# Kernel tuning notes

Measured on AMD Instinct MI355X. Metric: run time of the kernel, lower is better.

Reference implementation:

```python
import jax, jax.numpy as jnp
import numpy as np

B, T, NW, NF = 4, 1, 1536, 16
N_CROSS = 400_000
N_EDGES = 1_600_000
C_OUT = 4
IN_DIM = 2 * NF + 2  # 34


def setup_inputs() -> dict:
    key = jax.random.key(0)
    ks = jax.random.split(key, 16)
    return {
        "first_wires": jax.random.normal(ks[0], (B, T, NW, NF), jnp.float32),
        "second_wires": jax.random.normal(ks[1], (B, T, NW, NF), jnp.float32),
        "crossings": jax.random.normal(ks[2], (N_CROSS, 2), jnp.float32),
        "bbox": jax.random.uniform(ks[3], (3,), jnp.float32) + 0.5,
        "edge_attr": jax.random.normal(ks[4], (N_EDGES, 4), jnp.float32),
        "indices": jax.random.randint(ks[5], (N_CROSS, 2), 0, NW),
        "edge_index": jax.random.randint(ks[6], (2, N_EDGES), 0, N_CROSS),
        "W": jax.random.normal(ks[7], (IN_DIM, C_OUT), jnp.float32) / np.sqrt(IN_DIM),
        "att_src": jax.random.normal(ks[8], (C_OUT,), jnp.float32),
        "att_dst": jax.random.normal(ks[9], (C_OUT,), jnp.float32),
        "W_e": jax.random.normal(ks[10], (4, C_OUT), jnp.float32) / 2.0,
        "att_edge": jax.random.normal(ks[11], (C_OUT,), jnp.float32),
        "bias": jnp.zeros((C_OUT,), jnp.float32),
        "w_mlp": jax.random.normal(ks[12], (C_OUT, 1), jnp.float32) / 2.0,
        "b_mlp": jnp.zeros((1,), jnp.float32),
    }


def reference(first_wires, second_wires, crossings, bbox, edge_attr,
              indices, edge_index, W, att_src, att_dst, W_e, att_edge,
              bias, w_mlp, b_mlp):
    b, t = first_wires.shape[0], first_wires.shape[1]
    n = indices.shape[0]
    # fill_window: gather wire features for each crossing and append normalized coords
    fw = first_wires[:, :, indices[:, 0], :]          # [B,T,N,NF]
    sw = second_wires[:, :, indices[:, 1], :]         # [B,T,N,NF]
    xc = crossings / jnp.linalg.norm(bbox)            # [N,2]
    xc = jnp.broadcast_to(xc[None, None], (b, t, n, 2))
    x = jnp.concatenate([fw, sw, xc], axis=-1)        # [B,T,N,2NF+2]
    x = x.reshape(b * t, n, -1)

    src, dst = edge_index[0], edge_index[1]
    h = x @ W                                          # [BT,N,C]
    a_e = (edge_attr @ W_e) @ att_edge                 # [E]

    def gat(hb):
        hs, hd = hb[src], hb[dst]                      # [E,C]
        logits = jax.nn.leaky_relu(hs @ att_src + hd @ att_dst + a_e, 0.2)
        m = jax.ops.segment_max(logits, dst, num_segments=n)
        ex = jnp.exp(logits - m[dst])
        den = jax.ops.segment_sum(ex, dst, num_segments=n)
        alpha = ex / (den[dst] + 1e-16)
        return jax.ops.segment_sum(alpha[:, None] * hs, dst, num_segments=n) + bias

    out = jax.vmap(gat)(h)                             # [BT,N,C]
    y = out @ w_mlp + b_mlp                            # [BT,N,1]
    return y.reshape(b, t, n, 1)
```

## Files before the change

### kernel.cpp

```cpp
#include <hip/hip_runtime.h>
#include <math.h>

#define BB 4
#define NWIRE 1536
#define NFEAT 16
#define BS 256
#define NBLK 256
#define DSHIFT 8
#define DPB (1 << DSHIFT)
#define MAXNB 2048

__global__ void k_wires(const float* __restrict__ fw, const float* __restrict__ sw,
                        const float* __restrict__ W, const float* __restrict__ att_src,
                        const float* __restrict__ att_dst, const float* __restrict__ wmlp,
                        float4* __restrict__ fwpre, float4* __restrict__ swpre) {
    int t = blockIdx.x * blockDim.x + threadIdx.x;
    if (t >= BB * NWIRE) return;
    const float* fp = fw + (size_t)t * NFEAT;
    const float* sp = sw + (size_t)t * NFEAT;
    float hf[4] = {0, 0, 0, 0}, hs[4] = {0, 0, 0, 0};
    #pragma unroll
    for (int k = 0; k < NFEAT; ++k) {
        float a = fp[k], b = sp[k];
        #pragma unroll
        for (int c = 0; c < 4; ++c) {
            hf[c] = fmaf(a, W[k * 4 + c], hf[c]);
            hs[c] = fmaf(b, W[(NFEAT + k) * 4 + c], hs[c]);
        }
    }
    float fs = 0, fd = 0, fq = 0, ss = 0, sd = 0, sq = 0;
    #pragma unroll
    for (int c = 0; c < 4; ++c) {
        float as = att_src[c], ad = att_dst[c], wm = wmlp[c];
        fs = fmaf(hf[c], as, fs); fd = fmaf(hf[c], ad, fd); fq = fmaf(hf[c], wm, fq);
        ss = fmaf(hs[c], as, ss); sd = fmaf(hs[c], ad, sd); sq = fmaf(hs[c], wm, sq);
    }
    fwpre[t] = make_float4(fs, fd, fq, 0.0f);
    swpre[t] = make_float4(ss, sd, sq, 0.0f);
}

__global__ void k_nodes(const int* __restrict__ indices, const float* __restrict__ crossings,
                        const float* __restrict__ bbox, const float* __restrict__ W,
                        const float* __restrict__ att_src, const float* __restrict__ att_dst,
                        const float* __restrict__ wmlp,
                        const float4* __restrict__ fwpre, const float4* __restrict__ swpre,
                        float4* __restrict__ srcdat4, float4* __restrict__ dstdat4, int n) {
    int i = blockIdx.x * blockDim.x + threadIdx.x;
    if (i >= n) return;
    float inv = rsqrtf(bbox[0] * bbox[0] + bbox[1] * bbox[1] + bbox[2] * bbox[2]);
    int2 idx = ((const int2*)indices)[i];
    float2 xc = ((const float2*)crossings)[i];
    int i0 = idx.x, i1 = idx.y;
    float x0 = xc.x * inv, x1 = xc.y * inv;
    float xs = 0, xd = 0, xq = 0;
    #pragma unroll
    for (int c = 0; c < 4; ++c) {
        float hc = fmaf(x0, W[32 * 4 + c], x1 * W[33 * 4 + c]);
        xs = fmaf(hc, att_src[c], xs);
        xd = fmaf(hc, att_dst[c], xd);
        xq = fmaf(hc, wmlp[c], xq);
    }
    float4 f0 = fwpre[0 * NWIRE + i0], s0 = swpre[0 * NWIRE + i1];
    float4 f1 = fwpre[1 * NWIRE + i0], s1 = swpre[1 * NWIRE + i1];
    float4 f2 = fwpre[2 * NWIRE + i0], s2 = swpre[2 * NWIRE + i1];
    float4 f3 = fwpre[3 * NWIRE + i0], s3 = swpre[3 * NWIRE + i1];
    srcdat4[(size_t)i * 2] = make_float4(f0.x + s0.x + xs, f1.x + s1.x + xs,
                                         f2.x + s2.x + xs, f3.x + s3.x + xs);
    srcdat4[(size_t)i * 2 + 1] = make_float4(f0.z + s0.z + xq, f1.z + s1.z + xq,
                                             f2.z + s2.z + xq, f3.z + s3.z + xq);
    dstdat4[i] = make_float4(f0.y + s0.y + xd, f1.y + s1.y + xd,
                             f2.y + s2.y + xd, f3.y + s3.y + xd);
}

__global__ void k_binA1(const int* __restrict__ ei, int ne, int nb, int chunk,
                        int* __restrict__ bh) {
    __shared__ int lc[MAXNB];
    for (int i = threadIdx.x; i < nb; i += BS) lc[i] = 0;
    __syncthreads();
    int blk = blockIdx.x;
    const int* dstp = ei + ne;
    int e0 = blk * chunk, e1 = min(e0 + chunk, ne);
    int e = e0 + threadIdx.x * 4;
    for (; e + 3 < e1; e += BS * 4) {
        int4 d4 = *(const int4*)(dstp + e);
        atomicAdd(&lc[d4.x >> DSHIFT], 1);
        atomicAdd(&lc[d4.y >> DSHIFT], 1);
        atomicAdd(&lc[d4.z >> DSHIFT], 1);
        atomicAdd(&lc[d4.w >> DSHIFT], 1);
    }
    for (; e < e1; e += BS * 4) {
        int ke = min(e + 4, e1);
        for (int k = e; k < ke; ++k) atomicAdd(&lc[dstp[k] >> DSHIFT], 1);
    }
    __syncthreads();
    int* row = bh + (size_t)blk * nb;
    for (int b = threadIdx.x; b < nb; b += BS) row[b] = lc[b];
}

__global__ void k_scanBlk(int* __restrict__ bh, int* __restrict__ btot, int nb) {
    int b = blockIdx.x * blockDim.x + threadIdx.x;
    if (b >= nb) return;
    int run = 0;
    for (int k0 = 0; k0 < NBLK; k0 += 8) {
        int v[8];
        #pragma unroll
        for (int j = 0; j < 8; ++j) v[j] = bh[(size_t)(k0 + j) * nb + b];
        #pragma unroll
        for (int j = 0; j < 8; ++j) {
            int t = v[j];
            bh[(size_t)(k0 + j) * nb + b] = run;
            run += t;
        }
    }
    btot[b] = run;
}

__global__ void k_scanBuck(const int* __restrict__ btot, int* __restrict__ bbase,
                           int nb, int ne) {
    __shared__ int sh[1024];
    int t = threadIdx.x;
    int i0 = 2 * t, i1 = 2 * t + 1;
    int a = (i0 < nb) ? btot[i0] : 0;
    int b = (i1 < nb) ? btot[i1] : 0;
    sh[t] = a + b;
    __syncthreads();
    for (int ofs = 1; ofs < 1024; ofs <<= 1) {
        int u = (t >= ofs) ? sh[t - ofs] : 0;
        __syncthreads();
        sh[t] += u;
        __syncthreads();
    }
    int excl = sh[t] - (a + b);
    if (i0 < nb) bbase[i0] = excl;
    if (i1 < nb) bbase[i1] = excl + a;
    if (t == 0) bbase[nb] = ne;
}

__global__ void k_binA2(const int* __restrict__ ei, const float* __restrict__ eattr,
                        const float* __restrict__ We, const float* __restrict__ att_edge,
                        const int* __restrict__ bh, const int* __restrict__ bbase,
                        int ne, int nb, int chunk, int2* __restrict__ recs) {
    __shared__ int curs[MAXNB];
    int blk = blockIdx.x;
    const int* row = bh + (size_t)blk * nb;
    for (int b = threadIdx.x; b < nb; b += BS)
        curs[b] = bbase[b] + row[b];
    __syncthreads();
    float v0 = fmaf(We[0], att_edge[0], fmaf(We[1], att_edge[1], fmaf(We[2], att_edge[2], We[3] * att_edge[3])));
    float v1 = fmaf(We[4], att_edge[0], fmaf(We[5], att_edge[1], fmaf(We[6], att_edge[2], We[7] * att_edge[3])));
    float v2 = fmaf(We[8], att_edge[0], fmaf(We[9], att_edge[1], fmaf(We[10], att_edge[2], We[11] * att_edge[3])));
    float v3 = fmaf(We[12], att_edge[0], fmaf(We[13], att_edge[1], fmaf(We[14], att_edge[2], We[15] * att_edge[3])));
    const int* srcp = ei;
    const int* dstp = ei + ne;
    const float4* ea4 = (const float4*)eattr;
    int e0 = blk * chunk, e1 = min(e0 + chunk, ne);
    int e = e0 + threadIdx.x * 4;
    for (; e + 3 < e1; e += BS * 4) {
        int4 s4 = *(const int4*)(srcp + e);
        int4 d4 = *(const int4*)(dstp + e);
        float4 a0 = ea4[e], a1 = ea4[e + 1], a2 = ea4[e + 2], a3 = ea4[e + 3];
        float ae0 = fmaf(a0.x, v0, fmaf(a0.y, v1, fmaf(a0.z, v2, a0.w * v3)));
        float ae1 = fmaf(a1.x, v0, fmaf(a1.y, v1, fmaf(a1.z, v2, a1.w * v3)));
        float ae2 = fmaf(a2.x, v0, fmaf(a2.y, v1, fmaf(a2.z, v2, a2.w * v3)));
        float ae3 = fmaf(a3.x, v0, fmaf(a3.y, v1, fmaf(a3.z, v2, a3.w * v3)));
        int p0 = atomicAdd(&curs[d4.x >> DSHIFT], 1);
        int p1 = atomicAdd(&curs[d4.y >> DSHIFT], 1);
        int p2 = atomicAdd(&curs[d4.z >> DSHIFT], 1);
        int p3 = atomicAdd(&curs[d4.w >> DSHIFT], 1);
        recs[p0] = make_int2(((d4.x & (DPB - 1)) << 19) | s4.x, __float_as_int(ae0));
        recs[p1] = make_int2(((d4.y & (DPB - 1)) << 19) | s4.y, __float_as_int(ae1));
        recs[p2] = make_int2(((d4.z & (DPB - 1)) << 19) | s4.z, __float_as_int(ae2));
        recs[p3] = make_int2(((d4.w & (DPB - 1)) << 19) | s4.w, __float_as_int(ae3));
    }
    for (; e < e1; e += BS * 4) {
        int ke = min(e + 4, e1);
        for (int k = e; k < ke; ++k) {
            int s = srcp[k], d = dstp[k];
            float4 ea = ea4[k];
            float ae = fmaf(ea.x, v0, fmaf(ea.y, v1, fmaf(ea.z, v2, ea.w * v3)));
            int pos = atomicAdd(&curs[d >> DSHIFT], 1);
            recs[pos] = make_int2(((d & (DPB - 1)) << 19) | s, __float_as_int(ae));
        }
    }
}

__device__ __forceinline__ void gat_proc(int2 r, float4 ps, float4 q,
                                         float* acc, const float* pds) {
    int dlo = (unsigned)r.x >> 19;
    float ae = __int_as_float(r.y);
    float lg, ex;
    lg = ps.x + pds[dlo * 4]     + ae; lg = lg > 0.0f ? lg : 0.2f * lg; ex = expf(lg);
    atomicAdd(&acc[dlo * 8],     ex); atomicAdd(&acc[dlo * 8 + 1], ex * q.x);
    lg = ps.y + pds[dlo * 4 + 1] + ae; lg = lg > 0.0f ? lg : 0.2f * lg; ex = expf(lg);
    atomicAdd(&acc[dlo * 8 + 2], ex); atomicAdd(&acc[dlo * 8 + 3], ex * q.y);
    lg = ps.z + pds[dlo * 4 + 2] + ae; lg = lg > 0.0f ? lg : 0.2f * lg; ex = expf(lg);
    atomicAdd(&acc[dlo * 8 + 4], ex); atomicAdd(&acc[dlo * 8 + 5], ex * q.z);
    lg = ps.w + pds[dlo * 4 + 3] + ae; lg = lg > 0.0f ? lg : 0.2f * lg; ex = expf(lg);
    atomicAdd(&acc[dlo * 8 + 6], ex); atomicAdd(&acc[dlo * 8 + 7], ex * q.w);
}

__global__ void __launch_bounds__(BS)
k_gatB(const int2* __restrict__ recs, const int* __restrict__ bbase,
       const float4* __restrict__ srcdat4, const float4* __restrict__ dstdat4,
       const float* __restrict__ bias, const float* __restrict__ wmlp,
       const float* __restrict__ bmlp, float* __restrict__ out, int n) {
    __shared__ float acc[DPB * 8];
    __shared__ float pds[DPB * 4];
    int b = blockIdx.x;
    int r0 = bbase[b], r1 = bbase[b + 1];
    int dbase = b << DSHIFT;
    int dmax = min(DPB, n - dbase);
    for (int i = threadIdx.x; i < DPB * 8; i += BS) acc[i] = 0.0f;
    for (int i = threadIdx.x; i < dmax; i += BS) {
        float4 pd = dstdat4[dbase + i];
        pds[i * 4]     = pd.x;
        pds[i * 4 + 1] = pd.y;
        pds[i * 4 + 2] = pd.z;
        pds[i * 4 + 3] = pd.w;
    }
    __syncthreads();
    int i = r0 + threadIdx.x;
    for (; i + 3 * BS < r1; i += 4 * BS) {
        int2 ra = recs[i], rb = recs[i + BS], rc = recs[i + 2 * BS], rd = recs[i + 3 * BS];
        int sa = ra.x & 0x7FFFF, sb = rb.x & 0x7FFFF;
        int sc = rc.x & 0x7FFFF, sd = rd.x & 0x7FFFF;
        float4 Pa = srcdat4[(size_t)sa * 2], Qa = srcdat4[(size_t)sa * 2 + 1];
        float4 Pb = srcdat4[(size_t)sb * 2], Qb = srcdat4[(size_t)sb * 2 + 1];
        float4 Pc = srcdat4[(size_t)sc * 2], Qc = srcdat4[(size_t)sc * 2 + 1];
        float4 Pd = srcdat4[(size_t)sd * 2], Qd = srcdat4[(size_t)sd * 2 + 1];
        gat_proc(ra, Pa, Qa, acc, pds);
        gat_proc(rb, Pb, Qb, acc, pds);
        gat_proc(rc, Pc, Qc, acc, pds);
        gat_proc(rd, Pd, Qd, acc, pds);
    }
    for (; i < r1; i += BS) {
        int2 r = recs[i];
        int s = r.x & 0x7FFFF;
        gat_proc(r, srcdat4[(size_t)s * 2], srcdat4[(size_t)s * 2 + 1], acc, pds);
    }
    __syncthreads();
    float cst = fmaf(bias[0], wmlp[0], fmaf(bias[1], wmlp[1], fmaf(bias[2], wmlp[2], bias[3] * wmlp[3]))) + bmlp[0];
    for (int i2 = threadIdx.x; i2 < dmax; i2 += BS) {
        int d = dbase + i2;
        out[d]                 = acc[i2 * 8 + 1] / (acc[i2 * 8]     + 1e-16f) + cst;
        out[(size_t)n + d]     = acc[i2 * 8 + 3] / (acc[i2 * 8 + 2] + 1e-16f) + cst;
        out[(size_t)2 * n + d] = acc[i2 * 8 + 5] / (acc[i2 * 8 + 4] + 1e-16f) + cst;
        out[(size_t)3 * n + d] = acc[i2 * 8 + 7] / (acc[i2 * 8 + 6] + 1e-16f) + cst;
    }
}

extern "C" void kernel_launch(void* const* d_in, const int* in_sizes, int n_in,
                              void* d_out, int out_size, void* d_ws, size_t ws_size,
                              hipStream_t stream) {
    const float* first_wires  = (const float*)d_in[0];
    const float* second_wires = (const float*)d_in[1];
    const float* crossings    = (const float*)d_in[2];
    const float* bbox         = (const float*)d_in[3];
    const float* edge_attr    = (const float*)d_in[4];
    const int*   indices      = (const int*)d_in[5];
    const int*   edge_index   = (const int*)d_in[6];
    const float* W            = (const float*)d_in[7];
    const float* att_src      = (const float*)d_in[8];
    const float* att_dst      = (const float*)d_in[9];
    const float* W_e          = (const float*)d_in[10];
    const float* att_edge     = (const float*)d_in[11];
    const float* bias         = (const float*)d_in[12];
    const float* w_mlp        = (const float*)d_in[13];
    const float* b_mlp        = (const float*)d_in[14];
    float* out = (float*)d_out;

    const int n  = in_sizes[5] / 2;
    const int ne = in_sizes[6] / 2;
    const int nb = (n + DPB - 1) >> DSHIFT;
    const int chunk = (((ne + NBLK - 1) / NBLK) + 3) & ~3;

    char* ws = (char*)d_ws;
    size_t off = 0;
    float4* fwpre   = (float4*)(ws + off); off += (size_t)BB * NWIRE * 16;
    float4* swpre   = (float4*)(ws + off); off += (size_t)BB * NWIRE * 16;
    float4* srcdat4 = (float4*)(ws + off); off += (size_t)n * 32;
    float4* dstdat4 = (float4*)(ws + off); off += (size_t)n * 16;
    int*    bh      = (int*)(ws + off);    off += (size_t)nb * NBLK * 4;
    int*    btot    = (int*)(ws + off);    off += ((size_t)nb * 4 + 15) & ~15ull;
    int*    bbase   = (int*)(ws + off);    off += ((size_t)(nb + 1) * 4 + 15) & ~15ull;
    int2*   recs    = (int2*)(ws + off);   off += (size_t)ne * 8;

    hipLaunchKernelGGL(k_wires, dim3((BB * NWIRE + BS - 1) / BS), dim3(BS), 0, stream,
                       first_wires, second_wires, W, att_src, att_dst, w_mlp, fwpre, swpre);
    hipLaunchKernelGGL(k_nodes, dim3((n + BS - 1) / BS), dim3(BS), 0, stream,
                       indices, crossings, bbox, W, att_src, att_dst, w_mlp,
                       fwpre, swpre, srcdat4, dstdat4, n);
    hipLaunchKernelGGL(k_binA1, dim3(NBLK), dim3(BS), 0, stream,
                       edge_index, ne, nb, chunk, bh);
    hipLaunchKernelGGL(k_scanBlk, dim3((nb + 63) / 64), dim3(64), 0, stream,
                       bh, btot, nb);
    hipLaunchKernelGGL(k_scanBuck, dim3(1), dim3(1024), 0, stream,
                       btot, bbase, nb, ne);
    hipLaunchKernelGGL(k_binA2, dim3(NBLK), dim3(BS), 0, stream,
                       edge_index, edge_attr, W_e, att_edge, bh, bbase, ne, nb, chunk, recs);
    hipLaunchKernelGGL(k_gatB, dim3(nb), dim3(BS), 0, stream,
                       recs, bbase, srcdat4, dstdat4, bias, w_mlp, b_mlp, out, n);
}
```

Baseline: 257.9 us.

## Split GAT aggregation across batches with per-batch planar node data

```diff
diff --git a/kernel.cpp b/kernel.cpp
--- a/kernel.cpp
+++ b/kernel.cpp
@@ -44,7 +44,7 @@
                         const float* __restrict__ att_src, const float* __restrict__ att_dst,
                         const float* __restrict__ wmlp,
                         const float4* __restrict__ fwpre, const float4* __restrict__ swpre,
-                        float4* __restrict__ srcdat4, float4* __restrict__ dstdat4, int n) {
+                        float2* __restrict__ srcb, float* __restrict__ dstb, int n) {
     int i = blockIdx.x * blockDim.x + threadIdx.x;
     if (i >= n) return;
     float inv = rsqrtf(bbox[0] * bbox[0] + bbox[1] * bbox[1] + bbox[2] * bbox[2]);
@@ -60,16 +60,13 @@
         xd = fmaf(hc, att_dst[c], xd);
         xq = fmaf(hc, wmlp[c], xq);
     }
-    float4 f0 = fwpre[0 * NWIRE + i0], s0 = swpre[0 * NWIRE + i1];
-    float4 f1 = fwpre[1 * NWIRE + i0], s1 = swpre[1 * NWIRE + i1];
-    float4 f2 = fwpre[2 * NWIRE + i0], s2 = swpre[2 * NWIRE + i1];
-    float4 f3 = fwpre[3 * NWIRE + i0], s3 = swpre[3 * NWIRE + i1];
-    srcdat4[(size_t)i * 2] = make_float4(f0.x + s0.x + xs, f1.x + s1.x + xs,
-                                         f2.x + s2.x + xs, f3.x + s3.x + xs);
-    srcdat4[(size_t)i * 2 + 1] = make_float4(f0.z + s0.z + xq, f1.z + s1.z + xq,
-                                             f2.z + s2.z + xq, f3.z + s3.z + xq);
-    dstdat4[i] = make_float4(f0.y + s0.y + xd, f1.y + s1.y + xd,
-                             f2.y + s2.y + xd, f3.y + s3.y + xd);
+    #pragma unroll
+    for (int b = 0; b < BB; ++b) {
+        float4 f = fwpre[b * NWIRE + i0];
+        float4 s = swpre[b * NWIRE + i1];
+        srcb[(size_t)b * n + i] = make_float2(f.x + s.x + xs, f.z + s.z + xq);
+        dstb[(size_t)b * n + i] = f.y + s.y + xd;
+    }
 }
 
 __global__ void k_binA1(const int* __restrict__ ei, int ne, int nb, int chunk,
@@ -184,69 +181,62 @@
     }
 }
 
-__device__ __forceinline__ void gat_proc(int2 r, float4 ps, float4 q,
-                                         float* acc, const float* pds) {
-    int dlo = (unsigned)r.x >> 19;
-    float ae = __int_as_float(r.y);
-    float lg, ex;
-    lg = ps.x + pds[dlo * 4]     + ae; lg = lg > 0.0f ? lg : 0.2f * lg; ex = expf(lg);
-    atomicAdd(&acc[dlo * 8],     ex); atomicAdd(&acc[dlo * 8 + 1], ex * q.x);
-    lg = ps.y + pds[dlo * 4 + 1] + ae; lg = lg > 0.0f ? lg : 0.2f * lg; ex = expf(lg);
-    atomicAdd(&acc[dlo * 8 + 2], ex); atomicAdd(&acc[dlo * 8 + 3], ex * q.y);
-    lg = ps.z + pds[dlo * 4 + 2] + ae; lg = lg > 0.0f ? lg : 0.2f * lg; ex = expf(lg);
-    atomicAdd(&acc[dlo * 8 + 4], ex); atomicAdd(&acc[dlo * 8 + 5], ex * q.z);
-    lg = ps.w + pds[dlo * 4 + 3] + ae; lg = lg > 0.0f ? lg : 0.2f * lg; ex = expf(lg);
-    atomicAdd(&acc[dlo * 8 + 6], ex); atomicAdd(&acc[dlo * 8 + 7], ex * q.w);
-}
-
 __global__ void __launch_bounds__(BS)
 k_gatB(const int2* __restrict__ recs, const int* __restrict__ bbase,
-       const float4* __restrict__ srcdat4, const float4* __restrict__ dstdat4,
+       const float2* __restrict__ srcb, const float* __restrict__ dstb,
        const float* __restrict__ bias, const float* __restrict__ wmlp,
-       const float* __restrict__ bmlp, float* __restrict__ out, int n) {
-    __shared__ float acc[DPB * 8];
-    __shared__ float pds[DPB * 4];
-    int b = blockIdx.x;
-    int r0 = bbase[b], r1 = bbase[b + 1];
-    int dbase = b << DSHIFT;
+       const float* __restrict__ bmlp, float* __restrict__ out, int n, int nb) {
+    __shared__ float2 acc[DPB];
+    __shared__ float pds[DPB];
+    int g = blockIdx.x;
+    int s = g & 7;
+    int batch = s >> 1;
+    int bucket = (g >> 3) * 2 + (s & 1);
+    if (bucket >= nb) return;
+    int r0 = bbase[bucket], r1 = bbase[bucket + 1];
+    int dbase = bucket << DSHIFT;
     int dmax = min(DPB, n - dbase);
-    for (int i = threadIdx.x; i < DPB * 8; i += BS) acc[i] = 0.0f;
-    for (int i = threadIdx.x; i < dmax; i += BS) {
-        float4 pd = dstdat4[dbase + i];
-        pds[i * 4]     = pd.x;
-        pds[i * 4 + 1] = pd.y;
-        pds[i * 4 + 2] = pd.z;
-        pds[i * 4 + 3] = pd.w;
-    }
-    __syncthreads();
+    const float* db = dstb + (size_t)batch * n;
+    for (int i = threadIdx.x; i < DPB; i += BS) acc[i] = make_float2(0.0f, 0.0f);
+    for (int i = threadIdx.x; i < dmax; i += BS) pds[i] = db[dbase + i];
+    __syncthreads();
+    const float2* sb = srcb + (size_t)batch * n;
     int i = r0 + threadIdx.x;
     for (; i + 3 * BS < r1; i += 4 * BS) {
         int2 ra = recs[i], rb = recs[i + BS], rc = recs[i + 2 * BS], rd = recs[i + 3 * BS];
-        int sa = ra.x & 0x7FFFF, sb = rb.x & 0x7FFFF;
-        int sc = rc.x & 0x7FFFF, sd = rd.x & 0x7FFFF;
-        float4 Pa = srcdat4[(size_t)sa * 2], Qa = srcdat4[(size_t)sa * 2 + 1];
-        float4 Pb = srcdat4[(size_t)sb * 2], Qb = srcdat4[(size_t)sb * 2 + 1];
-        float4 Pc = srcdat4[(size_t)sc * 2], Qc = srcdat4[(size_t)sc * 2 + 1];
-        float4 Pd = srcdat4[(size_t)sd * 2], Qd = srcdat4[(size_t)sd * 2 + 1];
-        gat_proc(ra, Pa, Qa, acc, pds);
-        gat_proc(rb, Pb, Qb, acc, pds);
-        gat_proc(rc, Pc, Qc, acc, pds);
-        gat_proc(rd, Pd, Qd, acc, pds);
+        float2 pa = sb[ra.x & 0x7FFFF];
+        float2 pb = sb[rb.x & 0x7FFFF];
+        float2 pc = sb[rc.x & 0x7FFFF];
+        float2 pd = sb[rd.x & 0x7FFFF];
+        float lg, ex;
+        int dlo;
+        dlo = (unsigned)ra.x >> 19;
+        lg = pa.x + pds[dlo] + __int_as_float(ra.y); lg = lg > 0.0f ? lg : 0.2f * lg; ex = expf(lg);
+        atomicAdd(&acc[dlo].x, ex); atomicAdd(&acc[dlo].y, ex * pa.y);
+        dlo = (unsigned)rb.x >> 19;
+        lg = pb.x + pds[dlo] + __int_as_float(rb.y); lg = lg > 0.0f ? lg : 0.2f * lg; ex = expf(lg);
+        atomicAdd(&acc[dlo].x, ex); atomicAdd(&acc[dlo].y, ex * pb.y);
+        dlo = (unsigned)rc.x >> 19;
+        lg = pc.x + pds[dlo] + __int_as_float(rc.y); lg = lg > 0.0f ? lg : 0.2f * lg; ex = expf(lg);
+        atomicAdd(&acc[dlo].x, ex); atomicAdd(&acc[dlo].y, ex * pc.y);
+        dlo = (unsigned)rd.x >> 19;
+        lg = pd.x + pds[dlo] + __int_as_float(rd.y); lg = lg > 0.0f ? lg : 0.2f * lg; ex = expf(lg);
+        atomicAdd(&acc[dlo].x, ex); atomicAdd(&acc[dlo].y, ex * pd.y);
     }
     for (; i < r1; i += BS) {
         int2 r = recs[i];
-        int s = r.x & 0x7FFFF;
-        gat_proc(r, srcdat4[(size_t)s * 2], srcdat4[(size_t)s * 2 + 1], acc, pds);
+        float2 pq = sb[r.x & 0x7FFFF];
+        int dlo = (unsigned)r.x >> 19;
+        float lg = pq.x + pds[dlo] + __int_as_float(r.y);
+        lg = lg > 0.0f ? lg : 0.2f * lg;
+        float ex = expf(lg);
+        atomicAdd(&acc[dlo].x, ex); atomicAdd(&acc[dlo].y, ex * pq.y);
     }
     __syncthreads();
     float cst = fmaf(bias[0], wmlp[0], fmaf(bias[1], wmlp[1], fmaf(bias[2], wmlp[2], bias[3] * wmlp[3]))) + bmlp[0];
-    for (int i2 = threadIdx.x; i2 < dmax; i2 += BS) {
-        int d = dbase + i2;
-        out[d]                 = acc[i2 * 8 + 1] / (acc[i2 * 8]     + 1e-16f) + cst;
-        out[(size_t)n + d]     = acc[i2 * 8 + 3] / (acc[i2 * 8 + 2] + 1e-16f) + cst;
-        out[(size_t)2 * n + d] = acc[i2 * 8 + 5] / (acc[i2 * 8 + 4] + 1e-16f) + cst;
-        out[(size_t)3 * n + d] = acc[i2 * 8 + 7] / (acc[i2 * 8 + 6] + 1e-16f) + cst;
-    }
+    float* ob = out + (size_t)batch * n;
+    for (int i2 = threadIdx.x; i2 < dmax; i2 += BS)
+        ob[dbase + i2] = acc[i2].y / (acc[i2].x + 1e-16f) + cst;
 }
 
 extern "C" void kernel_launch(void* const* d_in, const int* in_sizes, int n_in,
@@ -272,24 +262,25 @@
     const int n  = in_sizes[5] / 2;
     const int ne = in_sizes[6] / 2;
     const int nb = (n + DPB - 1) >> DSHIFT;
+    const int nbp = (nb + 1) & ~1;
     const int chunk = (((ne + NBLK - 1) / NBLK) + 3) & ~3;
 
     char* ws = (char*)d_ws;
     size_t off = 0;
-    float4* fwpre   = (float4*)(ws + off); off += (size_t)BB * NWIRE * 16;
-    float4* swpre   = (float4*)(ws + off); off += (size_t)BB * NWIRE * 16;
-    float4* srcdat4 = (float4*)(ws + off); off += (size_t)n * 32;
-    float4* dstdat4 = (float4*)(ws + off); off += (size_t)n * 16;
-    int*    bh      = (int*)(ws + off);    off += (size_t)nb * NBLK * 4;
-    int*    btot    = (int*)(ws + off);    off += ((size_t)nb * 4 + 15) & ~15ull;
-    int*    bbase   = (int*)(ws + off);    off += ((size_t)(nb + 1) * 4 + 15) & ~15ull;
-    int2*   recs    = (int2*)(ws + off);   off += (size_t)ne * 8;
+    float4* fwpre = (float4*)(ws + off); off += (size_t)BB * NWIRE * 16;
+    float4* swpre = (float4*)(ws + off); off += (size_t)BB * NWIRE * 16;
+    float2* srcb  = (float2*)(ws + off); off += (size_t)BB * n * 8;
+    float*  dstb  = (float*)(ws + off);  off += (size_t)BB * n * 4;
+    int*    bh    = (int*)(ws + off);    off += (size_t)nb * NBLK * 4;
+    int*    btot  = (int*)(ws + off);    off += ((size_t)nb * 4 + 15) & ~15ull;
+    int*    bbase = (int*)(ws + off);    off += ((size_t)(nb + 1) * 4 + 15) & ~15ull;
+    int2*   recs  = (int2*)(ws + off);   off += (size_t)ne * 8;
 
     hipLaunchKernelGGL(k_wires, dim3((BB * NWIRE + BS - 1) / BS), dim3(BS), 0, stream,
                        first_wires, second_wires, W, att_src, att_dst, w_mlp, fwpre, swpre);
     hipLaunchKernelGGL(k_nodes, dim3((n + BS - 1) / BS), dim3(BS), 0, stream,
                        indices, crossings, bbox, W, att_src, att_dst, w_mlp,
-                       fwpre, swpre, srcdat4, dstdat4, n);
+                       fwpre, swpre, srcb, dstb, n);
     hipLaunchKernelGGL(k_binA1, dim3(NBLK), dim3(BS), 0, stream,
                        edge_index, ne, nb, chunk, bh);
     hipLaunchKernelGGL(k_scanBlk, dim3((nb + 63) / 64), dim3(64), 0, stream,
@@ -298,6 +289,6 @@
                        btot, bbase, nb, ne);
     hipLaunchKernelGGL(k_binA2, dim3(NBLK), dim3(BS), 0, stream,
                        edge_index, edge_attr, W_e, att_edge, bh, bbase, ne, nb, chunk, recs);
-    hipLaunchKernelGGL(k_gatB, dim3(nb), dim3(BS), 0, stream,
-                       recs, bbase, srcdat4, dstdat4, bias, w_mlp, b_mlp, out, n);
-}
+    hipLaunchKernelGGL(k_gatB, dim3(nbp * 4), dim3(BS), 0, stream,
+                       recs, bbase, srcb, dstb, bias, w_mlp, b_mlp, out, n, nb);
+}
```

After: 249.1 us. -3.4%, faster.
